# Optimization experiments

Measured on AMD Instinct MI355X. Metric: run time of the kernel, lower is better.

The kernel has to match this reference:

```python
import jax, jax.numpy as jnp
import numpy as np

N_QUBITS = 14
N_LAYERS = 3
BATCH = 256


def _apply_1q(state, U, q, n):
    # state: (B, 2^n) flat; apply 2x2 gate U on qubit q.
    # U: (2,2) shared or (B,2,2) per-sample.
    B = state.shape[0]
    s = state.reshape(B, 2 ** q, 2, 2 ** (n - 1 - q))
    if U.ndim == 3:
        s = jnp.einsum('bij,bajc->baic', U, s)
    else:
        s = jnp.einsum('ij,bajc->baic', U, s)
    return s.reshape(B, -1)


def _apply_cnot(state, c, t, n):
    # CNOT: |c, t> -> |c, t xor c>. Flip target axis on the control=1 block.
    B = state.shape[0]
    a, b = (c, t) if c < t else (t, c)
    s = state.reshape(B, 2 ** a, 2, 2 ** (b - a - 1), 2, 2 ** (n - 1 - b))
    c_ax = 2 if c < t else 4
    t_ax = 4 if c < t else 2
    s0 = jax.lax.index_in_dim(s, 0, axis=c_ax, keepdims=False)
    s1 = jax.lax.index_in_dim(s, 1, axis=c_ax, keepdims=False)
    t_ax2 = t_ax if t_ax < c_ax else t_ax - 1
    s1 = jnp.flip(s1, axis=t_ax2)
    s = jnp.stack([s0, s1], axis=c_ax)
    return s.reshape(B, -1)


def _circuit(x, weights, n, L):
    # angles constrained to (-pi, pi) as in the torch wrapper
    angles = jnp.tanh(x) * jnp.float32(np.pi)  # (B, n)
    B = x.shape[0]
    state = jnp.zeros((B, 2 ** n), jnp.complex64).at[:, 0].set(1.0)
    # AngleEmbedding with RY rotations (per-sample gate matrices)
    for q in range(n):
        th = angles[:, q] * 0.5
        c, s = jnp.cos(th), jnp.sin(th)
        U = jnp.stack([jnp.stack([c, -s], -1), jnp.stack([s, c], -1)], -2)
        state = _apply_1q(state, U.astype(jnp.complex64), q, n)
    # BasicEntanglerLayers: per layer, RX(w) on each wire then CNOT ring
    for l in range(L):
        for q in range(n):
            th = weights[l, q] * 0.5
            c = jnp.cos(th).astype(jnp.complex64)
            s = jnp.sin(th).astype(jnp.complex64)
            mis = jnp.complex64(-1j) * s
            U = jnp.stack([jnp.stack([c, mis]), jnp.stack([mis, c])])
            state = _apply_1q(state, U, q, n)
        num_cnots = n if n > 2 else (1 if n == 2 else 0)
        for q in range(num_cnots):
            state = _apply_cnot(state, q, (q + 1) % n, n)
    # <Z_q> = P(q=0) - P(q=1)
    p = (jnp.abs(state) ** 2).reshape((B,) + (2,) * n)  # float32 probs
    expvals = []
    for q in range(n):
        pq = jnp.sum(p, axis=tuple(a for a in range(1, n + 1) if a != q + 1))
        expvals.append(pq[:, 0] - pq[:, 1])
    return jnp.stack(expvals, axis=-1)  # (B, n)


def setup_inputs() -> dict:
    key = jax.random.key(0)
    kx, kw = jax.random.split(key)
    x = jax.random.normal(kx, (BATCH, N_QUBITS), jnp.float32)
    # TorchLayer default init for BasicEntanglerLayers: uniform in [0, 2*pi)
    weights = jax.random.uniform(kw, (N_LAYERS, N_QUBITS), jnp.float32, 0.0, 2.0 * np.pi)
    return {"x": x, "weights": weights}


def reference(x, weights):
    return _circuit(x, weights, N_QUBITS, N_LAYERS)
```

## Files before the change

kernel.cpp:

```cpp
#include <hip/hip_runtime.h>
#include <math.h>

#define NQ 14
#define DIM (1 << NQ)
#define NT 512
#define TA 32
#define NW (NT / 64)
#define PDIM (DIM + DIM / 32)

template <int J> struct IC { static constexpr int v = J; };
template <int N, typename F>
__device__ __forceinline__ void sfor(F&& f) {
    if constexpr (N > 0) { sfor<N - 1>(f); f(IC<N - 1>{}); }
}

typedef float cf2 __attribute__((ext_vector_type(2)));

__device__ __forceinline__ cf2 pk_mul_c(cf2 cs, cf2 a) {
    cf2 t;
    asm("v_pk_mul_f32 %0, %1, %2 op_sel:[0,0] op_sel_hi:[0,1]"
        : "=v"(t) : "v"(cs), "v"(a));
    return t;
}
__device__ __forceinline__ cf2 pk_mul_s(cf2 cs, cf2 a) {
    cf2 t;
    asm("v_pk_mul_f32 %0, %1, %2 op_sel:[1,0] op_sel_hi:[1,1]"
        : "=v"(t) : "v"(cs), "v"(a));
    return t;
}
__device__ __forceinline__ cf2 pk_mul_s_swapneg(cf2 cs, cf2 a) {
    cf2 t;
    asm("v_pk_mul_f32 %0, %1, %2 op_sel:[1,1] op_sel_hi:[1,0] neg_hi:[0,1]"
        : "=v"(t) : "v"(cs), "v"(a));
    return t;
}
__device__ __forceinline__ cf2 pk_fma_c(cf2 cs, cf2 a, cf2 b) {
    cf2 d;
    asm("v_pk_fma_f32 %0, %1, %2, %3 op_sel:[0,0,0] op_sel_hi:[0,1,1]"
        : "=v"(d) : "v"(cs), "v"(a), "v"(b));
    return d;
}
__device__ __forceinline__ cf2 pk_fma_s(cf2 cs, cf2 a, cf2 b) {
    cf2 d;
    asm("v_pk_fma_f32 %0, %1, %2, %3 op_sel:[1,0,0] op_sel_hi:[1,1,1]"
        : "=v"(d) : "v"(cs), "v"(a), "v"(b));
    return d;
}
__device__ __forceinline__ cf2 pk_fma_c_nb(cf2 cs, cf2 a, cf2 b) {
    cf2 d;
    asm("v_pk_fma_f32 %0, %1, %2, %3 op_sel:[0,0,0] op_sel_hi:[0,1,1] neg_lo:[0,0,1] neg_hi:[0,0,1]"
        : "=v"(d) : "v"(cs), "v"(a), "v"(b));
    return d;
}

struct St {
    cf2 a0, a1, a2, a3, a4, a5, a6, a7, a8, a9, a10, a11, a12, a13, a14, a15,
        a16, a17, a18, a19, a20, a21, a22, a23, a24, a25, a26, a27, a28, a29, a30, a31;
};
template <int J> __device__ __forceinline__ cf2& amp(St& s);
#define AMP_GET(J) template <> __device__ __forceinline__ cf2& amp<J>(St& s) { return s.a##J; }
AMP_GET(0)  AMP_GET(1)  AMP_GET(2)  AMP_GET(3)  AMP_GET(4)  AMP_GET(5)  AMP_GET(6)  AMP_GET(7)
AMP_GET(8)  AMP_GET(9)  AMP_GET(10) AMP_GET(11) AMP_GET(12) AMP_GET(13) AMP_GET(14) AMP_GET(15)
AMP_GET(16) AMP_GET(17) AMP_GET(18) AMP_GET(19) AMP_GET(20) AMP_GET(21) AMP_GET(22) AMP_GET(23)
AMP_GET(24) AMP_GET(25) AMP_GET(26) AMP_GET(27) AMP_GET(28) AMP_GET(29) AMP_GET(30) AMP_GET(31)

__host__ __device__ constexpr int pad(int idx) { return idx + (idx >> 5); }

template <int P0, int P1, int P2, int P3, int P4>
struct Tile5 {
    static constexpr int PMASK = (1 << P0) | (1 << P1) | (1 << P2) | (1 << P3) | (1 << P4);
    static __device__ __forceinline__ int base_idx(int t) {
        int idx = 0, tb = 0;
#pragma unroll
        for (int p = 0; p < NQ; ++p)
            if (!((PMASK >> p) & 1)) { idx |= ((t >> tb) & 1) << p; ++tb; }
        return idx;
    }
    static constexpr int off(int j) {
        return ((j & 1) << P0) | (((j >> 1) & 1) << P1) | (((j >> 2) & 1) << P2) |
               (((j >> 3) & 1) << P3) | (((j >> 4) & 1) << P4);
    }
    static constexpr int poff(int j) { return pad(off(j)); }
};

using TT1 = Tile5<9, 10, 11, 12, 13>;
using TT2 = Tile5<4, 5, 6, 7, 8>;
using TT3 = Tile5<13, 0, 1, 2, 3>;

template <class T>
__device__ __forceinline__ void load_tile(const cf2* s, int pb, St& st) {
    sfor<TA>([&](auto jc) {
        constexpr int j = decltype(jc)::v;
        amp<j>(st) = s[pb + T::poff(j)];
    });
}
template <class T>
__device__ __forceinline__ void load_tile_fold(const cf2* s, int pbLo, int pbHi, St& st) {
    sfor<TA>([&](auto jc) {
        constexpr int j = decltype(jc)::v;
        amp<j>(st) = s[((j & 16) ? pbHi : pbLo) + T::poff(j)];
    });
}
template <class T>
__device__ __forceinline__ void store_tile(cf2* s, int pb, St& st) {
    sfor<TA>([&](auto jc) {
        constexpr int j = decltype(jc)::v;
        s[pb + T::poff(j)] = amp<j>(st);
    });
}

template <int LB>
__device__ __forceinline__ void g_ry(St& st, cf2 cs) {
    sfor<TA>([&](auto jc) {
        constexpr int j = decltype(jc)::v;
        if constexpr (!(j & (1 << LB))) {
            constexpr int k = j | (1 << LB);
            cf2 aj = amp<j>(st), ak = amp<k>(st);
            amp<j>(st) = pk_fma_c_nb(cs, aj, pk_mul_s(cs, ak));
            amp<k>(st) = pk_fma_s(cs, aj, pk_mul_c(cs, ak));
        }
    });
}
template <int LB>
__device__ __forceinline__ void g_rx(St& st, cf2 cs) {
    sfor<TA>([&](auto jc) {
        constexpr int j = decltype(jc)::v;
        if constexpr (!(j & (1 << LB))) {
            constexpr int k = j | (1 << LB);
            cf2 aj = amp<j>(st), ak = amp<k>(st);
            amp<j>(st) = pk_fma_c(cs, aj, pk_mul_s_swapneg(cs, ak));
            amp<k>(st) = pk_fma_c(cs, ak, pk_mul_s_swapneg(cs, aj));
        }
    });
}
template <int LC, int LT>
__device__ __forceinline__ void g_cnot(St& st) {
    sfor<TA>([&](auto jc) {
        constexpr int j = decltype(jc)::v;
        if constexpr (((j >> LC) & 1) && !((j >> LT) & 1)) {
            constexpr int k = j | (1 << LT);
            cf2 t = amp<j>(st);
            amp<j>(st) = amp<k>(st);
            amp<k>(st) = t;
        }
    });
}
template <int LT>
__device__ __forceinline__ void g_cnot_pred(St& st, bool ctrl) {
    sfor<TA>([&](auto jc) {
        constexpr int j = decltype(jc)::v;
        if constexpr (!((j >> LT) & 1)) {
            constexpr int k = j | (1 << LT);
            cf2 a = amp<j>(st), b = amp<k>(st);
            amp<j>(st) = ctrl ? b : a;
            amp<k>(st) = ctrl ? a : b;
        }
    });
}

__global__ void __launch_bounds__(NT) qsim_kernel(const float* __restrict__ x,
                                                  const float* __restrict__ w,
                                                  float* __restrict__ out) {
    __shared__ cf2 sSt[PDIM];
    __shared__ cf2 sCS[56];
    __shared__ float sRed[NW][NQ];

    const int tid = threadIdx.x;
    const int b = blockIdx.x;

    if (tid < 14) {
        float th = tanhf(x[b * NQ + tid]) * 1.57079632679489662f;
        cf2 v; v.x = cosf(th); v.y = sinf(th);
        sCS[tid] = v;
    } else if (tid < 56) {
        float th = w[tid - 14] * 0.5f;
        cf2 v; v.x = cosf(th); v.y = sinf(th);
        sCS[tid] = v;
    }

    const int pbT1 = pad(TT1::base_idx(tid));
    const int pbT2 = pad(TT2::base_idx(tid));
    const int pbT3 = pad(TT3::base_idx(tid));
    const int d2 = ((tid >> 4) & 1) ? 264 : 0;
    const int pbT2lo = pbT2 + d2, pbT2hi = pbT2 - d2;
    const int d3 = (tid & 1) ? 8 : 0;
    const int pbT3lo = pbT3 + d3, pbT3hi = pbT3 - d3;

    const bool c45 = (tid >> 4) & 1;
    const bool c9A = tid & 1;

    __syncthreads();

    St st;

    {
        sfor<TA>([&](auto jc) {
            constexpr int j = decltype(jc)::v;
            cf2 z; z.x = 0.f; z.y = 0.f;
            amp<j>(st) = z;
        });
        if (tid == 0) amp<0>(st).x = 1.f;
        g_ry<0>(st, sCS[4]); g_ry<1>(st, sCS[3]); g_ry<2>(st, sCS[2]);
        g_ry<3>(st, sCS[1]); g_ry<4>(st, sCS[0]);
        g_rx<0>(st, sCS[18]); g_rx<1>(st, sCS[17]); g_rx<2>(st, sCS[16]);
        g_rx<3>(st, sCS[15]); g_rx<4>(st, sCS[14]);
        g_cnot<4, 3>(st); g_cnot<3, 2>(st); g_cnot<2, 1>(st); g_cnot<1, 0>(st);
        store_tile<TT1>(sSt, pbT1, st);
    }
    __syncthreads();
    {
        cf2 y5 = sCS[5], y6 = sCS[6], y7 = sCS[7], y8 = sCS[8], y9 = sCS[9];
        cf2 x5 = sCS[19], x6 = sCS[20], x7 = sCS[21], x8 = sCS[22], x9 = sCS[23];
        load_tile<TT2>(sSt, pbT2, st);
        g_ry<0>(st, y9); g_ry<1>(st, y8); g_ry<2>(st, y7); g_ry<3>(st, y6); g_ry<4>(st, y5);
        g_rx<0>(st, x9); g_rx<1>(st, x8); g_rx<2>(st, x7); g_rx<3>(st, x6); g_rx<4>(st, x5);
        g_cnot_pred<4>(st, c45);
        g_cnot<4, 3>(st); g_cnot<3, 2>(st); g_cnot<2, 1>(st); g_cnot<1, 0>(st);
        store_tile<TT2>(sSt, pbT2, st);
    }
    __syncthreads();
    {
        cf2 yA = sCS[10], yB = sCS[11], yC = sCS[12], yD = sCS[13];
        cf2 xA = sCS[24], xB = sCS[25], xC = sCS[26], xD = sCS[27];
        load_tile<TT3>(sSt, pbT3, st);
        g_ry<1>(st, yD); g_ry<2>(st, yC); g_ry<3>(st, yB); g_ry<4>(st, yA);
        g_rx<1>(st, xD); g_rx<2>(st, xC); g_rx<3>(st, xB); g_rx<4>(st, xA);
        g_cnot_pred<4>(st, c9A);
        g_cnot<4, 3>(st); g_cnot<3, 2>(st); g_cnot<2, 1>(st); g_cnot<1, 0>(st);
        store_tile<TT3>(sSt, pbT3, st);
    }
    __syncthreads();

#pragma unroll 1
    for (int l = 1; l < 3; ++l) {
        const int s0 = 14 + l * NQ;
        {
            cf2 c0 = sCS[s0 + 0], c1 = sCS[s0 + 1], c2 = sCS[s0 + 2];
            cf2 c3 = sCS[s0 + 3], c4 = sCS[s0 + 4];
            load_tile<TT1>(sSt, pbT1, st);
            g_rx<0>(st, c4); g_rx<1>(st, c3); g_rx<2>(st, c2);
            g_rx<3>(st, c1); g_rx<4>(st, c0);
            g_cnot<4, 3>(st); g_cnot<3, 2>(st); g_cnot<2, 1>(st); g_cnot<1, 0>(st);
            store_tile<TT1>(sSt, pbT1, st);
        }
        __syncthreads();
        {
            cf2 c5 = sCS[s0 + 5], c6 = sCS[s0 + 6], c7 = sCS[s0 + 7];
            cf2 c8 = sCS[s0 + 8], c9 = sCS[s0 + 9];
            load_tile_fold<TT2>(sSt, pbT2lo, pbT2hi, st);
            g_rx<0>(st, c9); g_rx<1>(st, c8); g_rx<2>(st, c7);
            g_rx<3>(st, c6); g_rx<4>(st, c5);
            g_cnot<4, 3>(st); g_cnot<3, 2>(st); g_cnot<2, 1>(st); g_cnot<1, 0>(st);
            store_tile<TT2>(sSt, pbT2, st);
        }
        __syncthreads();
        {
            cf2 cA = sCS[s0 + 10], cB = sCS[s0 + 11], cC = sCS[s0 + 12], cD = sCS[s0 + 13];
            load_tile_fold<TT3>(sSt, pbT3lo, pbT3hi, st);
            g_rx<1>(st, cD); g_rx<2>(st, cC); g_rx<3>(st, cB); g_rx<4>(st, cA);
            g_cnot<4, 3>(st); g_cnot<3, 2>(st); g_cnot<2, 1>(st); g_cnot<1, 0>(st);
            if (l == 1) store_tile<TT3>(sSt, pbT3, st);
        }
        if (l == 1) __syncthreads();
    }

    float Stot = 0.f, S0 = 0.f, S1 = 0.f, S2 = 0.f, S3 = 0.f, S4 = 0.f;
    sfor<TA>([&](auto jc) {
        constexpr int j = decltype(jc)::v;
        cf2 v = amp<j>(st);
        float pj = v.x * v.x + v.y * v.y;
        Stot += pj;
        S0 += (j & 1)  ? -pj : pj;
        S1 += (j & 2)  ? -pj : pj;
        S2 += (j & 4)  ? -pj : pj;
        S3 += (j & 8)  ? -pj : pj;
        S4 += (j & 16) ? -pj : pj;
    });
    float ev[NQ];
    ev[0] = S0; ev[10] = S4; ev[11] = S3; ev[12] = S2; ev[13] = S1;
#pragma unroll
    for (int q = 1; q <= 9; ++q)
        ev[q] = ((tid >> (9 - q)) & 1) ? -Stot : Stot;

#pragma unroll
    for (int q = 0; q < NQ; ++q) {
#pragma unroll
        for (int o = 32; o > 0; o >>= 1) ev[q] += __shfl_down(ev[q], o);
    }
    const int wv = tid >> 6, ln = tid & 63;
    if (ln == 0) {
#pragma unroll
        for (int q = 0; q < NQ; ++q) sRed[wv][q] = ev[q];
    }
    __syncthreads();
    if (tid < NQ) {
        float acc = 0.f;
#pragma unroll
        for (int k = 0; k < NW; ++k) acc += sRed[k][tid];
        out[b * NQ + tid] = acc;
    }
}

extern "C" void kernel_launch(void* const* d_in, const int* in_sizes, int n_in,
                              void* d_out, int out_size, void* d_ws, size_t ws_size,
                              hipStream_t stream) {
    const float* x = (const float*)d_in[0];
    const float* w = (const float*)d_in[1];
    float* out = (float*)d_out;
    qsim_kernel<<<256, NT, 0, stream>>>(x, w, out);
}
```

Before: 78.28 us.

## Compute first-layer product state analytically and split tile gate stages into halves

The first tile stage is replaced by a closed-form product-state amplitude for qubits 0-4. The RY, RX and CNOT chain on those qubits acting on |0> gives a single nonzero amplitude per thread, so one shared-memory pass and barrier are skipped. Gate application in each stage is reordered: the top-bit gate runs first, then each half of the register tile is processed and stored independently so stores can overlap remaining compute. Load order is interleaved to match. This adds per-thread scalar setup and changes register scheduling, which may affect register pressure.

```diff
diff --git a/kernel.cpp b/kernel.cpp
--- a/kernel.cpp
+++ b/kernel.cpp
@@ -90,22 +90,24 @@
 template <class T>
 __device__ __forceinline__ void load_tile(const cf2* s, int pb, St& st) {
     sfor<TA>([&](auto jc) {
-        constexpr int j = decltype(jc)::v;
+        constexpr int j0 = decltype(jc)::v;
+        constexpr int j = (j0 >> 1) | ((j0 & 1) << 4);
         amp<j>(st) = s[pb + T::poff(j)];
     });
 }
 template <class T>
 __device__ __forceinline__ void load_tile_fold(const cf2* s, int pbLo, int pbHi, St& st) {
     sfor<TA>([&](auto jc) {
-        constexpr int j = decltype(jc)::v;
+        constexpr int j0 = decltype(jc)::v;
+        constexpr int j = (j0 >> 1) | ((j0 & 1) << 4);
         amp<j>(st) = s[((j & 16) ? pbHi : pbLo) + T::poff(j)];
     });
 }
-template <class T>
-__device__ __forceinline__ void store_tile(cf2* s, int pb, St& st) {
-    sfor<TA>([&](auto jc) {
-        constexpr int j = decltype(jc)::v;
-        s[pb + T::poff(j)] = amp<j>(st);
+template <class T, int HI>
+__device__ __forceinline__ void store_half(cf2* s, int pb, St& st) {
+    sfor<TA>([&](auto jc) {
+        constexpr int j = decltype(jc)::v;
+        if constexpr ((j >> 4) == HI) s[pb + T::poff(j)] = amp<j>(st);
     });
 }
 
@@ -133,11 +135,35 @@
         }
     });
 }
-template <int LC, int LT>
-__device__ __forceinline__ void g_cnot(St& st) {
-    sfor<TA>([&](auto jc) {
-        constexpr int j = decltype(jc)::v;
-        if constexpr (((j >> LC) & 1) && !((j >> LT) & 1)) {
+template <int LB, int HI>
+__device__ __forceinline__ void g_ry_h(St& st, cf2 cs) {
+    sfor<TA>([&](auto jc) {
+        constexpr int j = decltype(jc)::v;
+        if constexpr (!(j & (1 << LB)) && ((j >> 4) == HI)) {
+            constexpr int k = j | (1 << LB);
+            cf2 aj = amp<j>(st), ak = amp<k>(st);
+            amp<j>(st) = pk_fma_c_nb(cs, aj, pk_mul_s(cs, ak));
+            amp<k>(st) = pk_fma_s(cs, aj, pk_mul_c(cs, ak));
+        }
+    });
+}
+template <int LB, int HI>
+__device__ __forceinline__ void g_rx_h(St& st, cf2 cs) {
+    sfor<TA>([&](auto jc) {
+        constexpr int j = decltype(jc)::v;
+        if constexpr (!(j & (1 << LB)) && ((j >> 4) == HI)) {
+            constexpr int k = j | (1 << LB);
+            cf2 aj = amp<j>(st), ak = amp<k>(st);
+            amp<j>(st) = pk_fma_c(cs, aj, pk_mul_s_swapneg(cs, ak));
+            amp<k>(st) = pk_fma_c(cs, ak, pk_mul_s_swapneg(cs, aj));
+        }
+    });
+}
+template <int LC, int LT, int HI>
+__device__ __forceinline__ void g_cnot_h(St& st) {
+    sfor<TA>([&](auto jc) {
+        constexpr int j = decltype(jc)::v;
+        if constexpr (((j >> LC) & 1) && !((j >> LT) & 1) && ((j >> 4) == HI)) {
             constexpr int k = j | (1 << LT);
             cf2 t = amp<j>(st);
             amp<j>(st) = amp<k>(st);
@@ -194,40 +220,57 @@
     St st;
 
     {
+        cf2 y5 = sCS[5], y6 = sCS[6], y7 = sCS[7], y8 = sCS[8], y9 = sCS[9];
+        cf2 x5 = sCS[19], x6 = sCS[20], x7 = sCS[21], x8 = sCS[22], x9 = sCS[23];
+
+        const int B0 = (tid >> 8) & 1, B1 = (tid >> 7) & 1, B2 = (tid >> 6) & 1,
+                  B3 = (tid >> 5) & 1, B4 = (tid >> 4) & 1;
+        const int bb0 = B0, bb1 = B1 ^ B0, bb2 = B2 ^ B1, bb3 = B3 ^ B2, bb4 = B4 ^ B3;
+        const int bb[5] = {bb0, bb1, bb2, bb3, bb4};
+        float pr = 1.f, pi = 0.f;
+#pragma unroll
+        for (int q = 0; q < 5; ++q) {
+            cf2 ry = sCS[q], rx = sCS[14 + q];
+            float re = bb[q] ? rx.x * ry.y : rx.x * ry.x;
+            float im = bb[q] ? -rx.y * ry.x : -rx.y * ry.y;
+            float nr = pr * re - pi * im;
+            pi = pr * im + pi * re;
+            pr = nr;
+        }
+        const bool act = (tid & 15) == 0;
+
         sfor<TA>([&](auto jc) {
             constexpr int j = decltype(jc)::v;
             cf2 z; z.x = 0.f; z.y = 0.f;
             amp<j>(st) = z;
         });
-        if (tid == 0) amp<0>(st).x = 1.f;
-        g_ry<0>(st, sCS[4]); g_ry<1>(st, sCS[3]); g_ry<2>(st, sCS[2]);
-        g_ry<3>(st, sCS[1]); g_ry<4>(st, sCS[0]);
-        g_rx<0>(st, sCS[18]); g_rx<1>(st, sCS[17]); g_rx<2>(st, sCS[16]);
-        g_rx<3>(st, sCS[15]); g_rx<4>(st, sCS[14]);
-        g_cnot<4, 3>(st); g_cnot<3, 2>(st); g_cnot<2, 1>(st); g_cnot<1, 0>(st);
-        store_tile<TT1>(sSt, pbT1, st);
-    }
-    __syncthreads();
-    {
-        cf2 y5 = sCS[5], y6 = sCS[6], y7 = sCS[7], y8 = sCS[8], y9 = sCS[9];
-        cf2 x5 = sCS[19], x6 = sCS[20], x7 = sCS[21], x8 = sCS[22], x9 = sCS[23];
-        load_tile<TT2>(sSt, pbT2, st);
-        g_ry<0>(st, y9); g_ry<1>(st, y8); g_ry<2>(st, y7); g_ry<3>(st, y6); g_ry<4>(st, y5);
-        g_rx<0>(st, x9); g_rx<1>(st, x8); g_rx<2>(st, x7); g_rx<3>(st, x6); g_rx<4>(st, x5);
-        g_cnot_pred<4>(st, c45);
-        g_cnot<4, 3>(st); g_cnot<3, 2>(st); g_cnot<2, 1>(st); g_cnot<1, 0>(st);
-        store_tile<TT2>(sSt, pbT2, st);
+        amp<0>(st).x = act ? pr : 0.f;
+        amp<0>(st).y = act ? pi : 0.f;
+
+        g_ry<4>(st, y5); g_rx<4>(st, x5); g_cnot_pred<4>(st, c45);
+        g_ry_h<3,0>(st, y6); g_ry_h<2,0>(st, y7); g_ry_h<1,0>(st, y8); g_ry_h<0,0>(st, y9);
+        g_rx_h<3,0>(st, x6); g_rx_h<2,0>(st, x7); g_rx_h<1,0>(st, x8); g_rx_h<0,0>(st, x9);
+        g_cnot_h<3,2,0>(st); g_cnot_h<2,1,0>(st); g_cnot_h<1,0,0>(st);
+        store_half<TT2, 0>(sSt, pbT2, st);
+        g_ry_h<3,1>(st, y6); g_ry_h<2,1>(st, y7); g_ry_h<1,1>(st, y8); g_ry_h<0,1>(st, y9);
+        g_rx_h<3,1>(st, x6); g_rx_h<2,1>(st, x7); g_rx_h<1,1>(st, x8); g_rx_h<0,1>(st, x9);
+        g_cnot_h<4,3,1>(st); g_cnot_h<3,2,1>(st); g_cnot_h<2,1,1>(st); g_cnot_h<1,0,1>(st);
+        store_half<TT2, 1>(sSt, pbT2, st);
     }
     __syncthreads();
     {
         cf2 yA = sCS[10], yB = sCS[11], yC = sCS[12], yD = sCS[13];
         cf2 xA = sCS[24], xB = sCS[25], xC = sCS[26], xD = sCS[27];
         load_tile<TT3>(sSt, pbT3, st);
-        g_ry<1>(st, yD); g_ry<2>(st, yC); g_ry<3>(st, yB); g_ry<4>(st, yA);
-        g_rx<1>(st, xD); g_rx<2>(st, xC); g_rx<3>(st, xB); g_rx<4>(st, xA);
-        g_cnot_pred<4>(st, c9A);
-        g_cnot<4, 3>(st); g_cnot<3, 2>(st); g_cnot<2, 1>(st); g_cnot<1, 0>(st);
-        store_tile<TT3>(sSt, pbT3, st);
+        g_ry<4>(st, yA); g_rx<4>(st, xA); g_cnot_pred<4>(st, c9A);
+        g_ry_h<3,0>(st, yB); g_ry_h<2,0>(st, yC); g_ry_h<1,0>(st, yD);
+        g_rx_h<3,0>(st, xB); g_rx_h<2,0>(st, xC); g_rx_h<1,0>(st, xD);
+        g_cnot_h<3,2,0>(st); g_cnot_h<2,1,0>(st); g_cnot_h<1,0,0>(st);
+        store_half<TT3, 0>(sSt, pbT3, st);
+        g_ry_h<3,1>(st, yB); g_ry_h<2,1>(st, yC); g_ry_h<1,1>(st, yD);
+        g_rx_h<3,1>(st, xB); g_rx_h<2,1>(st, xC); g_rx_h<1,1>(st, xD);
+        g_cnot_h<4,3,1>(st); g_cnot_h<3,2,1>(st); g_cnot_h<2,1,1>(st); g_cnot_h<1,0,1>(st);
+        store_half<TT3, 1>(sSt, pbT3, st);
     }
     __syncthreads();
 
@@ -238,28 +281,38 @@
             cf2 c0 = sCS[s0 + 0], c1 = sCS[s0 + 1], c2 = sCS[s0 + 2];
             cf2 c3 = sCS[s0 + 3], c4 = sCS[s0 + 4];
             load_tile<TT1>(sSt, pbT1, st);
-            g_rx<0>(st, c4); g_rx<1>(st, c3); g_rx<2>(st, c2);
-            g_rx<3>(st, c1); g_rx<4>(st, c0);
-            g_cnot<4, 3>(st); g_cnot<3, 2>(st); g_cnot<2, 1>(st); g_cnot<1, 0>(st);
-            store_tile<TT1>(sSt, pbT1, st);
+            g_rx<4>(st, c0);
+            g_rx_h<3,0>(st, c1); g_rx_h<2,0>(st, c2); g_rx_h<1,0>(st, c3); g_rx_h<0,0>(st, c4);
+            g_cnot_h<3,2,0>(st); g_cnot_h<2,1,0>(st); g_cnot_h<1,0,0>(st);
+            store_half<TT1, 0>(sSt, pbT1, st);
+            g_rx_h<3,1>(st, c1); g_rx_h<2,1>(st, c2); g_rx_h<1,1>(st, c3); g_rx_h<0,1>(st, c4);
+            g_cnot_h<4,3,1>(st); g_cnot_h<3,2,1>(st); g_cnot_h<2,1,1>(st); g_cnot_h<1,0,1>(st);
+            store_half<TT1, 1>(sSt, pbT1, st);
         }
         __syncthreads();
         {
             cf2 c5 = sCS[s0 + 5], c6 = sCS[s0 + 6], c7 = sCS[s0 + 7];
             cf2 c8 = sCS[s0 + 8], c9 = sCS[s0 + 9];
             load_tile_fold<TT2>(sSt, pbT2lo, pbT2hi, st);
-            g_rx<0>(st, c9); g_rx<1>(st, c8); g_rx<2>(st, c7);
-            g_rx<3>(st, c6); g_rx<4>(st, c5);
-            g_cnot<4, 3>(st); g_cnot<3, 2>(st); g_cnot<2, 1>(st); g_cnot<1, 0>(st);
-            store_tile<TT2>(sSt, pbT2, st);
+            g_rx<4>(st, c5);
+            g_rx_h<3,0>(st, c6); g_rx_h<2,0>(st, c7); g_rx_h<1,0>(st, c8); g_rx_h<0,0>(st, c9);
+            g_cnot_h<3,2,0>(st); g_cnot_h<2,1,0>(st); g_cnot_h<1,0,0>(st);
+            store_half<TT2, 0>(sSt, pbT2, st);
+            g_rx_h<3,1>(st, c6); g_rx_h<2,1>(st, c7); g_rx_h<1,1>(st, c8); g_rx_h<0,1>(st, c9);
+            g_cnot_h<4,3,1>(st); g_cnot_h<3,2,1>(st); g_cnot_h<2,1,1>(st); g_cnot_h<1,0,1>(st);
+            store_half<TT2, 1>(sSt, pbT2, st);
         }
         __syncthreads();
         {
             cf2 cA = sCS[s0 + 10], cB = sCS[s0 + 11], cC = sCS[s0 + 12], cD = sCS[s0 + 13];
             load_tile_fold<TT3>(sSt, pbT3lo, pbT3hi, st);
-            g_rx<1>(st, cD); g_rx<2>(st, cC); g_rx<3>(st, cB); g_rx<4>(st, cA);
-            g_cnot<4, 3>(st); g_cnot<3, 2>(st); g_cnot<2, 1>(st); g_cnot<1, 0>(st);
-            if (l == 1) store_tile<TT3>(sSt, pbT3, st);
+            g_rx<4>(st, cA);
+            g_rx_h<3,0>(st, cB); g_rx_h<2,0>(st, cC); g_rx_h<1,0>(st, cD);
+            g_cnot_h<3,2,0>(st); g_cnot_h<2,1,0>(st); g_cnot_h<1,0,0>(st);
+            if (l == 1) store_half<TT3, 0>(sSt, pbT3, st);
+            g_rx_h<3,1>(st, cB); g_rx_h<2,1>(st, cC); g_rx_h<1,1>(st, cD);
+            g_cnot_h<4,3,1>(st); g_cnot_h<3,2,1>(st); g_cnot_h<2,1,1>(st); g_cnot_h<1,0,1>(st);
+            if (l == 1) store_half<TT3, 1>(sSt, pbT3, st);
         }
         if (l == 1) __syncthreads();
     }
```

Measured after the change: 74.11 us. 5.3% less time.
